# Optimization experiments

Hardware: AMD Instinct MI355X
Metric: run time of the kernel (lower is better)

Reference implementation:

```python
import math
import jax, jax.numpy as jnp
import numpy as np

B, N, F_IN, F_H, F_OUT = 8, 2048, 128, 256, 256
RATIOS = (0.8, 0.5)
EDGE_P = 0.01  # adjacency density -> avg degree ~20


def setup_inputs() -> dict:
    key = jax.random.key(0)
    kx, ka, k1, k2, k3, k4, k5, k6 = jax.random.split(key, 8)
    x = jax.random.normal(kx, (B, N, F_IN), dtype=jnp.float32)
    u = jax.random.uniform(ka, (B, N, N), dtype=jnp.float32)
    # sparse nonneg weighted adjacency, zero diagonal (so gcn self-loop add == A + I)
    A = jnp.where(u < EDGE_P, u / EDGE_P, 0.0) * (1.0 - jnp.eye(N, dtype=jnp.float32))
    s_in, s_h = 1.0 / math.sqrt(F_IN), 1.0 / math.sqrt(F_H)
    W1 = jax.random.normal(k1, (F_IN, F_H), dtype=jnp.float32) * s_in
    b1 = jnp.zeros((F_H,), dtype=jnp.float32)
    p1 = jax.random.normal(k2, (F_H,), dtype=jnp.float32) * s_h
    W2 = jax.random.normal(k3, (F_H, F_OUT), dtype=jnp.float32) * s_h
    b2 = jnp.zeros((F_OUT,), dtype=jnp.float32)
    p2 = jax.random.normal(k4, (F_OUT,), dtype=jnp.float32) * s_h
    return {"x": x, "A": A, "W1": W1, "b1": b1, "p1": p1, "W2": W2, "b2": b2, "p2": p2}


def _gcn(x, A, W, b):
    # PyG GCNConv with gcn_norm: A_hat = A + I (diag(A)==0), deg = in-degree (col sums),
    # out[i] = sum_j dinv[j] * A_hat[j, i] * dinv[i] * (xW)[j] + b
    n = A.shape[0]
    A_hat = A + jnp.eye(n, dtype=A.dtype)
    dinv = jax.lax.rsqrt(A_hat.sum(axis=0))  # deg >= 1 due to self loops
    M = dinv[:, None] * A_hat * dinv[None, :]
    return M.T @ (x @ W) + b


def _topk_pool(x, A, p, k):
    # score = tanh(x @ p / ||p||); keep top-k nodes, scale features by score
    score = jnp.tanh((x @ p) / jnp.linalg.norm(p))
    vals, perm = jax.lax.top_k(score, k)
    return x[perm] * vals[:, None], A[perm][:, perm]


def _per_graph(x0, A0, W1, b1, p1, W2, b2, p2):
    n = x0.shape[0]
    k1 = math.ceil(RATIOS[0] * n)
    k2 = math.ceil(RATIOS[1] * k1)
    h = jax.nn.relu(_gcn(x0, A0, W1, b1))          # dropout is identity in eval mode
    h, A1 = _topk_pool(h, A0, p1, k1)
    h = jax.nn.relu(_gcn(h, A1, W2, b2))
    h, _ = _topk_pool(h, A1, p2, k2)
    # node_mask in the source is always all-True, so mean-fill never triggers:
    # rows [:k2] = pooled features, rest zeros.
    return jnp.zeros((n, h.shape[1]), dtype=h.dtype).at[:k2].set(h)


def reference(x, A, W1, b1, p1, W2, b2, p2):
    f = lambda xi, Ai: _per_graph(xi, Ai, W1, b1, p1, W2, b2, p2)
    return jax.vmap(f)(x, A)  # [B, N, F_OUT]
```

## Files before the change

### kernel.cpp

```cpp
#include <hip/hip_runtime.h>
#include <math.h>

#define BATCH 8
#define NN    2048
#define FIN   128
#define FH    256
#define KP1   1639
#define KP2   820
#define CAP   64

__global__ __launch_bounds__(256) void init_all(int* __restrict__ cnt,
                                                int* __restrict__ inv,
                                                const float* __restrict__ p1,
                                                const float* __restrict__ p2,
                                                double* __restrict__ norms) {
  int t = blockIdx.x * 256 + threadIdx.x;
  if (t < BATCH * NN) { cnt[t] = 0; inv[t] = -1; }
  if (blockIdx.x == 0) {
    __shared__ double red[256];
    int f = threadIdx.x;
    double v = (double)p1[f];
    red[f] = v * v;
    __syncthreads();
    for (int s = 128; s > 0; s >>= 1) { if (f < s) red[f] += red[f + s]; __syncthreads(); }
    if (f == 0) norms[0] = sqrt(red[0]);
    __syncthreads();
    v = (double)p2[f];
    red[f] = v * v;
    __syncthreads();
    for (int s = 128; s > 0; s >>= 1) { if (f < s) red[f] += red[f + s]; __syncthreads(); }
    if (f == 0) norms[1] = sqrt(red[0]);
  }
}

__global__ void build_csc1(const float* __restrict__ A, int* __restrict__ cnt,
                           int* __restrict__ idx, float* __restrict__ val) {
  const int total = BATCH * NN * (NN / 4);
  for (int t = blockIdx.x * blockDim.x + threadIdx.x; t < total;
       t += gridDim.x * blockDim.x) {
    float4 v4 = reinterpret_cast<const float4*>(A)[t];
    int b = t / (NN * NN / 4);
    int rem = t % (NN * NN / 4);
    int j = rem / (NN / 4);
    int i0 = (rem % (NN / 4)) * 4;
    float vv[4] = {v4.x, v4.y, v4.z, v4.w};
#pragma unroll
    for (int c = 0; c < 4; ++c) {
      float v = vv[c];
      if (v != 0.0f) {
        int col = b * NN + i0 + c;
        int p = atomicAdd(&cnt[col], 1);
        if (p < CAP) { idx[col * CAP + p] = j; val[col * CAP + p] = v; }
      }
    }
  }
}

__global__ __launch_bounds__(256) void canon_cols(int* __restrict__ cnt,
                                                  int* __restrict__ idx,
                                                  float* __restrict__ val,
                                                  double* __restrict__ dinv) {
  int wid = (blockIdx.x * blockDim.x + threadIdx.x) >> 6;
  int lane = threadIdx.x & 63;
  if (wid >= BATCH * NN) return;
  int c = cnt[wid]; if (c > CAP) c = CAP;
  if (lane == 0) cnt[wid] = c;
  int key = 0x7fffffff;
  float v = 0.0f;
  if (lane < c) {
    key = idx[(size_t)wid * CAP + lane];
    v = val[(size_t)wid * CAP + lane];
  }
#pragma unroll
  for (int k = 2; k <= 64; k <<= 1) {
#pragma unroll
    for (int j = k >> 1; j > 0; j >>= 1) {
      int pk = __shfl_xor(key, j);
      float pv = __shfl_xor(v, j);
      bool up = ((lane & k) == 0);
      bool takeMin = (((lane & j) == 0) == up);
      bool sw = takeMin ? (pk < key) : (pk > key);
      if (sw) { key = pk; v = pv; }
    }
  }
  if (lane < c) {
    idx[(size_t)wid * CAP + lane] = key;
    val[(size_t)wid * CAP + lane] = v;
  }
  double dv = (double)v;
#pragma unroll
  for (int off = 32; off > 0; off >>= 1) dv += __shfl_xor(dv, off);
  if (lane == 0) dinv[wid] = 1.0 / sqrt(1.0 + dv);
}

template <int KD, typename TX>
__global__ __launch_bounds__(512) void gemm_y(const TX* __restrict__ X,
                                              const float* __restrict__ W,
                                              const double* __restrict__ dinv,
                                              double* __restrict__ Y, int rows) {
  const int KC = 32;
  int b = blockIdx.y;
  int r0 = blockIdx.x * 32;
  int t = threadIdx.x;
  int fq = (t & 63) * 4;
  int rg = (t >> 6) * 4;
  __shared__ TX xs[32][KC];
  __shared__ float wsh[KC][FH];
  const TX* Xb = X + (size_t)b * NN * KD;
  double acc[4][4];
#pragma unroll
  for (int r = 0; r < 4; ++r)
#pragma unroll
    for (int c = 0; c < 4; ++c) acc[r][c] = 0.0;

  for (int kc = 0; kc < KD; kc += KC) {
    __syncthreads();
    for (int e = t; e < 32 * KC; e += 512) {
      int r = e >> 5, k = e & 31;
      int row = r0 + r;
      xs[r][k] = (row < rows) ? Xb[(size_t)row * KD + kc + k] : (TX)0;
    }
    for (int e = t; e < KC * FH / 4; e += 512) {
      int k = e >> 6;
      int f = (e << 2) & 255;
      *reinterpret_cast<float4*>(&wsh[k][f]) =
          *reinterpret_cast<const float4*>(&W[(size_t)(kc + k) * FH + f]);
    }
    __syncthreads();
#pragma unroll 2
    for (int k = 0; k < KC; k += 2) {
      float4 waf = *reinterpret_cast<const float4*>(&wsh[k][fq]);
      float4 wbf = *reinterpret_cast<const float4*>(&wsh[k + 1][fq]);
      double wa0 = (double)waf.x, wa1 = (double)waf.y;
      double wa2 = (double)waf.z, wa3 = (double)waf.w;
      double wb0 = (double)wbf.x, wb1 = (double)wbf.y;
      double wb2 = (double)wbf.z, wb3 = (double)wbf.w;
#pragma unroll
      for (int r = 0; r < 4; ++r) {
        double x0 = (double)xs[rg + r][k];
        double x1 = (double)xs[rg + r][k + 1];
        acc[r][0] = fma(x1, wb0, fma(x0, wa0, acc[r][0]));
        acc[r][1] = fma(x1, wb1, fma(x0, wa1, acc[r][1]));
        acc[r][2] = fma(x1, wb2, fma(x0, wa2, acc[r][2]));
        acc[r][3] = fma(x1, wb3, fma(x0, wa3, acc[r][3]));
      }
    }
  }
#pragma unroll
  for (int r = 0; r < 4; ++r) {
    int row = r0 + rg + r;
    if (row < rows) {
      double d = dinv[b * NN + row];
      double* o = Y + ((size_t)b * NN + row) * FH + fq;
      o[0] = d * acc[r][0];
      o[1] = d * acc[r][1];
      o[2] = d * acc[r][2];
      o[3] = d * acc[r][3];
    }
  }
}

__global__ __launch_bounds__(FH) void aggregate(
    const double* __restrict__ Y, const int* __restrict__ cnt,
    const int* __restrict__ idx, const float* __restrict__ val,
    const double* __restrict__ dinv, const float* __restrict__ bias,
    const float* __restrict__ p, double* __restrict__ H, double* __restrict__ dot) {
  int b = blockIdx.y, i = blockIdx.x, f = threadIdx.x;
  int col = b * NN + i;
  const int* ji = idx + (size_t)col * CAP;
  const float* jv = val + (size_t)col * CAP;
  const double* Yb = Y + (size_t)b * NN * FH;
  double acc = Y[(size_t)col * FH + f];
  int c = cnt[col];
  int a = 0;
  for (; a + 8 <= c; a += 8) {
    double tt[8];
    double vv[8];
#pragma unroll
    for (int u = 0; u < 8; ++u) {
      vv[u] = (double)jv[a + u];
      tt[u] = Yb[(size_t)ji[a + u] * FH + f];
    }
#pragma unroll
    for (int u = 0; u < 8; ++u) acc += vv[u] * tt[u];
  }
  for (; a < c; ++a) {
    acc += (double)jv[a] * Yb[(size_t)ji[a] * FH + f];
  }
  double h = fmax(dinv[col] * acc + (double)bias[f], 0.0);
  H[(size_t)col * FH + f] = h;
  double pd = h * (double)p[f];
#pragma unroll
  for (int off = 32; off > 0; off >>= 1) pd += __shfl_xor(pd, off);
  __shared__ double red[4];
  if ((f & 63) == 0) red[f >> 6] = pd;
  __syncthreads();
  if (f == 0) dot[col] = (red[0] + red[1]) + (red[2] + red[3]);
}

__global__ __launch_bounds__(1024) void topk_sort(
    const double* __restrict__ dot, const double* __restrict__ norms, int which,
    int valid, int k, int* __restrict__ perm, double* __restrict__ vals) {
  __shared__ double sk[NN];
  __shared__ int si[NN];
  int b = blockIdx.x, t = threadIdx.x;
  double nrm = norms[which];
  for (int e = t; e < NN; e += 1024) {
    sk[e] = (e < valid) ? tanh(dot[b * NN + e] / nrm) : -1.0e300;
    si[e] = e;
  }
  for (int kk = 2; kk <= NN; kk <<= 1) {
    for (int j = kk >> 1; j > 0; j >>= 1) {
      __syncthreads();
      int i = ((t & ~(j - 1)) << 1) | (t & (j - 1));
      int q = i | j;
      double ka = sk[i], kb = sk[q];
      int ia = si[i], ib = si[q];
      bool p_first = (kb > ka) || (kb == ka && ib < ia);
      bool up = ((i & kk) == 0);
      if (up ? p_first : !p_first) { sk[i] = kb; sk[q] = ka; si[i] = ib; si[q] = ia; }
    }
  }
  __syncthreads();
  for (int e = t; e < k; e += 1024) {
    perm[b * NN + e] = si[e];
    vals[b * NN + e] = sk[e];
  }
}

__global__ __launch_bounds__(FH) void pool1_kernel(
    const double* __restrict__ H, const int* __restrict__ perm,
    const double* __restrict__ vals, double* __restrict__ HP, int* __restrict__ inv) {
  int b = blockIdx.y, r = blockIdx.x, f = threadIdx.x;
  int node = perm[b * NN + r];
  double s = vals[b * NN + r];
  if (f == 0) inv[b * NN + node] = r;
  HP[((size_t)b * NN + r) * FH + f] = H[((size_t)b * NN + node) * FH + f] * s;
}

__global__ __launch_bounds__(256) void build_csc2(
    const int* __restrict__ cnt1, const int* __restrict__ idx1,
    const float* __restrict__ val1, const int* __restrict__ perm,
    const int* __restrict__ inv, int* __restrict__ cnt2, int* __restrict__ idx2,
    float* __restrict__ val2, double* __restrict__ dinv2) {
  int wid = (blockIdx.x * blockDim.x + threadIdx.x) >> 6;
  int lane = threadIdx.x & 63;
  if (wid >= BATCH * KP1) return;
  int b = wid / KP1, ri = wid % KP1;
  int colA = b * NN + perm[b * NN + ri];
  int c = cnt1[colA];
  int rj = -1;
  float v = 0.0f;
  if (lane < c) {
    int j = idx1[(size_t)colA * CAP + lane];
    v = val1[(size_t)colA * CAP + lane];
    rj = inv[b * NN + j];
  }
  bool keep = (lane < c) && (rj >= 0);
  unsigned long long mask = __ballot(keep);
  int pos = __popcll(mask & ((1ull << lane) - 1ull));
  int colB = b * NN + ri;
  if (keep) {
    idx2[(size_t)colB * CAP + pos] = rj;
    val2[(size_t)colB * CAP + pos] = v;
  }
  if (lane == 0) cnt2[colB] = (int)__popcll(mask);
  double dv = keep ? (double)v : 0.0;
#pragma unroll
  for (int off = 32; off > 0; off >>= 1) dv += __shfl_xor(dv, off);
  if (lane == 0) dinv2[colB] = 1.0 / sqrt(1.0 + dv);
}

__global__ __launch_bounds__(FH) void final_kernel(
    const double* __restrict__ H2, const int* __restrict__ perm2,
    const double* __restrict__ vals2, float* __restrict__ out) {
  int b = blockIdx.y, r = blockIdx.x, f = threadIdx.x;
  float o = 0.0f;
  if (r < KP2) {
    int rr = perm2[b * NN + r];
    o = (float)(H2[((size_t)b * NN + rr) * FH + f] * vals2[b * NN + r]);
  }
  out[((size_t)b * NN + r) * FH + f] = o;
}

extern "C" void kernel_launch(void* const* d_in, const int* in_sizes, int n_in,
                              void* d_out, int out_size, void* d_ws, size_t ws_size,
                              hipStream_t stream) {
  const float* x  = (const float*)d_in[0];
  const float* A  = (const float*)d_in[1];
  const float* W1 = (const float*)d_in[2];
  const float* b1 = (const float*)d_in[3];
  const float* p1 = (const float*)d_in[4];
  const float* W2 = (const float*)d_in[5];
  const float* b2 = (const float*)d_in[6];
  const float* p2 = (const float*)d_in[7];
  float* out = (float*)d_out;

  char* ws = (char*)d_ws;
  size_t off = 0;
  auto alloc = [&](size_t bytes) {
    void* p = ws + off;
    off += (bytes + 255) & ~(size_t)255;
    return p;
  };
  double* dot   = (double*)alloc((size_t)BATCH * NN * 8);
  double* y     = (double*)alloc((size_t)BATCH * NN * FH * 8);
  double* h     = (double*)alloc((size_t)BATCH * NN * FH * 8);
  double* hp    = (double*)alloc((size_t)BATCH * NN * FH * 8);
  double* dinv1 = (double*)alloc((size_t)BATCH * NN * 8);
  double* dinv2 = (double*)alloc((size_t)BATCH * NN * 8);
  int*   cnt1  = (int*)alloc((size_t)BATCH * NN * 4);
  int*   idx1  = (int*)alloc((size_t)BATCH * NN * CAP * 4);
  float* val1  = (float*)alloc((size_t)BATCH * NN * CAP * 4);
  int*   cnt2  = (int*)alloc((size_t)BATCH * NN * 4);
  int*   idx2  = (int*)alloc((size_t)BATCH * NN * CAP * 4);
  float* val2  = (float*)alloc((size_t)BATCH * NN * CAP * 4);
  int*   perm1 = (int*)alloc((size_t)BATCH * NN * 4);
  double* vals1 = (double*)alloc((size_t)BATCH * NN * 8);
  int*   perm2 = (int*)alloc((size_t)BATCH * NN * 4);
  double* vals2 = (double*)alloc((size_t)BATCH * NN * 8);
  int*   inv   = (int*)alloc((size_t)BATCH * NN * 4);
  double* norms = (double*)alloc(64);

  init_all<<<BATCH * NN / 256, 256, 0, stream>>>(cnt1, inv, p1, p2, norms);
  build_csc1<<<4096, 256, 0, stream>>>(A, cnt1, idx1, val1);
  canon_cols<<<(BATCH * NN * 64) / 256, 256, 0, stream>>>(cnt1, idx1, val1, dinv1);
  gemm_y<FIN, float><<<dim3(NN / 32, BATCH), 512, 0, stream>>>(x, W1, dinv1, y, NN);
  aggregate<<<dim3(NN, BATCH), FH, 0, stream>>>(y, cnt1, idx1, val1, dinv1, b1, p1, h, dot);
  topk_sort<<<BATCH, 1024, 0, stream>>>(dot, norms, 0, NN, KP1, perm1, vals1);
  pool1_kernel<<<dim3(KP1, BATCH), FH, 0, stream>>>(h, perm1, vals1, hp, inv);
  build_csc2<<<(BATCH * KP1 * 64 + 255) / 256, 256, 0, stream>>>(cnt1, idx1, val1, perm1,
                                                                 inv, cnt2, idx2, val2, dinv2);
  gemm_y<FH, double><<<dim3((KP1 + 31) / 32, BATCH), 512, 0, stream>>>(hp, W2, dinv2, y, KP1);
  aggregate<<<dim3(KP1, BATCH), FH, 0, stream>>>(y, cnt2, idx2, val2, dinv2, b2, p2, h, dot);
  topk_sort<<<BATCH, 1024, 0, stream>>>(dot, norms, 1, KP1, KP2, perm2, vals2);
  final_kernel<<<dim3(NN, BATCH), FH, 0, stream>>>(h, perm2, vals2, out);
}
```

Baseline: 323.1 us.

## Replace per-graph bitonic top-k with parallel rank counting; vectorize aggregate loads

The per-graph top-k, which ran as a single 1024-thread block doing a full bitonic sort, becomes a rank-by-counting kernel spread over many blocks per graph. Each element computes its rank by comparing against all raw dot scores in shared memory and scatters itself if it falls inside the top k. Since tanh is monotonic, ranking on raw dots is intended to give the same order, and tanh is now only applied to the kept elements. The aggregate kernel now uses double2 loads with 128 threads per column, halving the thread count and widening memory accesses. The cost is O(N^2) comparisons per graph in place of the sort, and a possible tie-ordering difference wherever tanh would have made distinct dots compare equal.

```diff
diff --git a/kernel.cpp b/kernel.cpp
--- a/kernel.cpp
+++ b/kernel.cpp
@@ -160,71 +160,74 @@
   }
 }
 
-__global__ __launch_bounds__(FH) void aggregate(
+__global__ __launch_bounds__(128) void aggregate(
     const double* __restrict__ Y, const int* __restrict__ cnt,
     const int* __restrict__ idx, const float* __restrict__ val,
     const double* __restrict__ dinv, const float* __restrict__ bias,
     const float* __restrict__ p, double* __restrict__ H, double* __restrict__ dot) {
-  int b = blockIdx.y, i = blockIdx.x, f = threadIdx.x;
+  int b = blockIdx.y, i = blockIdx.x, t = threadIdx.x;
   int col = b * NN + i;
+  int f0 = 2 * t;
   const int* ji = idx + (size_t)col * CAP;
   const float* jv = val + (size_t)col * CAP;
-  const double* Yb = Y + (size_t)b * NN * FH;
-  double acc = Y[(size_t)col * FH + f];
+  const double2* Yb = reinterpret_cast<const double2*>(Y + (size_t)b * NN * FH);
+  double2 s = Yb[(size_t)i * 128 + t];
+  double ax = s.x, ay = s.y;
   int c = cnt[col];
   int a = 0;
   for (; a + 8 <= c; a += 8) {
-    double tt[8];
+    double2 tt[8];
     double vv[8];
 #pragma unroll
     for (int u = 0; u < 8; ++u) {
       vv[u] = (double)jv[a + u];
-      tt[u] = Yb[(size_t)ji[a + u] * FH + f];
-    }
-#pragma unroll
-    for (int u = 0; u < 8; ++u) acc += vv[u] * tt[u];
+      tt[u] = Yb[(size_t)ji[a + u] * 128 + t];
+    }
+#pragma unroll
+    for (int u = 0; u < 8; ++u) { ax += vv[u] * tt[u].x; ay += vv[u] * tt[u].y; }
   }
   for (; a < c; ++a) {
-    acc += (double)jv[a] * Yb[(size_t)ji[a] * FH + f];
-  }
-  double h = fmax(dinv[col] * acc + (double)bias[f], 0.0);
-  H[(size_t)col * FH + f] = h;
-  double pd = h * (double)p[f];
+    double v = (double)jv[a];
+    double2 tt = Yb[(size_t)ji[a] * 128 + t];
+    ax += v * tt.x;
+    ay += v * tt.y;
+  }
+  double d = dinv[col];
+  double h0 = fmax(d * ax + (double)bias[f0], 0.0);
+  double h1 = fmax(d * ay + (double)bias[f0 + 1], 0.0);
+  reinterpret_cast<double2*>(H + (size_t)col * FH)[t] = make_double2(h0, h1);
+  double pd = h0 * (double)p[f0] + h1 * (double)p[f0 + 1];
 #pragma unroll
   for (int off = 32; off > 0; off >>= 1) pd += __shfl_xor(pd, off);
-  __shared__ double red[4];
-  if ((f & 63) == 0) red[f >> 6] = pd;
+  __shared__ double red[2];
+  if ((t & 63) == 0) red[t >> 6] = pd;
   __syncthreads();
-  if (f == 0) dot[col] = (red[0] + red[1]) + (red[2] + red[3]);
-}
-
-__global__ __launch_bounds__(1024) void topk_sort(
+  if (t == 0) dot[col] = red[0] + red[1];
+}
+
+__global__ __launch_bounds__(256) void topk_rank(
     const double* __restrict__ dot, const double* __restrict__ norms, int which,
-    int valid, int k, int* __restrict__ perm, double* __restrict__ vals) {
-  __shared__ double sk[NN];
-  __shared__ int si[NN];
-  int b = blockIdx.x, t = threadIdx.x;
-  double nrm = norms[which];
-  for (int e = t; e < NN; e += 1024) {
-    sk[e] = (e < valid) ? tanh(dot[b * NN + e] / nrm) : -1.0e300;
-    si[e] = e;
-  }
-  for (int kk = 2; kk <= NN; kk <<= 1) {
-    for (int j = kk >> 1; j > 0; j >>= 1) {
-      __syncthreads();
-      int i = ((t & ~(j - 1)) << 1) | (t & (j - 1));
-      int q = i | j;
-      double ka = sk[i], kb = sk[q];
-      int ia = si[i], ib = si[q];
-      bool p_first = (kb > ka) || (kb == ka && ib < ia);
-      bool up = ((i & kk) == 0);
-      if (up ? p_first : !p_first) { sk[i] = kb; sk[q] = ka; si[i] = ib; si[q] = ia; }
-    }
-  }
+    int valid, int kk, int* __restrict__ perm, double* __restrict__ vals) {
+  __shared__ double kd[NN];
+  int b = blockIdx.y, t = threadIdx.x;
+  for (int e = t; e < valid; e += 256) kd[e] = dot[b * NN + e];
   __syncthreads();
-  for (int e = t; e < k; e += 1024) {
-    perm[b * NN + e] = si[e];
-    vals[b * NN + e] = sk[e];
+  int e = blockIdx.x * 256 + t;
+  if (e >= valid) return;
+  double de = kd[e];
+  int rank = 0;
+  int j = 0;
+  for (; j + 4 <= valid; j += 4) {
+    double k0 = kd[j], k1 = kd[j + 1], k2 = kd[j + 2], k3 = kd[j + 3];
+    rank += (k0 > de) || (k0 == de && (j + 0) < e);
+    rank += (k1 > de) || (k1 == de && (j + 1) < e);
+    rank += (k2 > de) || (k2 == de && (j + 2) < e);
+    rank += (k3 > de) || (k3 == de && (j + 3) < e);
+  }
+  for (; j < valid; ++j) rank += (kd[j] > de) || (kd[j] == de && j < e);
+  if (rank < kk) {
+    perm[b * NN + rank] = e;
+    vals[b * NN + rank] = tanh(de / norms[which]);
   }
 }
 
@@ -326,13 +329,14 @@
   build_csc1<<<4096, 256, 0, stream>>>(A, cnt1, idx1, val1);
   canon_cols<<<(BATCH * NN * 64) / 256, 256, 0, stream>>>(cnt1, idx1, val1, dinv1);
   gemm_y<FIN, float><<<dim3(NN / 32, BATCH), 512, 0, stream>>>(x, W1, dinv1, y, NN);
-  aggregate<<<dim3(NN, BATCH), FH, 0, stream>>>(y, cnt1, idx1, val1, dinv1, b1, p1, h, dot);
-  topk_sort<<<BATCH, 1024, 0, stream>>>(dot, norms, 0, NN, KP1, perm1, vals1);
+  aggregate<<<dim3(NN, BATCH), 128, 0, stream>>>(y, cnt1, idx1, val1, dinv1, b1, p1, h, dot);
+  topk_rank<<<dim3(NN / 256, BATCH), 256, 0, stream>>>(dot, norms, 0, NN, KP1, perm1, vals1);
   pool1_kernel<<<dim3(KP1, BATCH), FH, 0, stream>>>(h, perm1, vals1, hp, inv);
   build_csc2<<<(BATCH * KP1 * 64 + 255) / 256, 256, 0, stream>>>(cnt1, idx1, val1, perm1,
                                                                  inv, cnt2, idx2, val2, dinv2);
   gemm_y<FH, double><<<dim3((KP1 + 31) / 32, BATCH), 512, 0, stream>>>(hp, W2, dinv2, y, KP1);
-  aggregate<<<dim3(KP1, BATCH), FH, 0, stream>>>(y, cnt2, idx2, val2, dinv2, b2, p2, h, dot);
-  topk_sort<<<BATCH, 1024, 0, stream>>>(dot, norms, 1, KP1, KP2, perm2, vals2);
+  aggregate<<<dim3(KP1, BATCH), 128, 0, stream>>>(y, cnt2, idx2, val2, dinv2, b2, p2, h, dot);
+  topk_rank<<<dim3((KP1 + 255) / 256, BATCH), 256, 0, stream>>>(dot, norms, 1, KP1, KP2,
+                                                                perm2, vals2);
   final_kernel<<<dim3(NN, BATCH), FH, 0, stream>>>(h, perm2, vals2, out);
 }
```

Measured after the change: 380.6 us. +17.8%, slower.
